# Kernel optimization log

Hardware: AMD Instinct MI355X
Metric: run time of the kernel (lower is better)

The kernel has to match this reference:

```python
import jax, jax.numpy as jnp
import numpy as np

B = 262144      # batch
DIN = 100       # input covariate dim (cfg_density[0][0])
H = 64          # hidden dim
G = 10          # num_grid -> density output dim G+1
NH = 5          # number of dosage-bucket heads in Multi_head


def setup_inputs() -> dict:
    key = jax.random.key(0)
    ks = jax.random.split(key, 16)
    s = 0.05
    return {
        "dosage": jax.random.uniform(ks[0], (B,), dtype=jnp.float32),
        "x": jax.random.normal(ks[1], (B, DIN), dtype=jnp.float32),
        # density feature MLP (two Linear+ReLU layers)
        "dW0": jax.random.normal(ks[2], (DIN, H), dtype=jnp.float32) * s,
        "db0": jax.random.normal(ks[3], (H,), dtype=jnp.float32) * s,
        "dW1": jax.random.normal(ks[4], (H, H), dtype=jnp.float32) * s,
        "db1": jax.random.normal(ks[5], (H,), dtype=jnp.float32) * s,
        # Density_Block: Linear(H -> G+1) then softmax + grid interpolation
        "dbW": jax.random.normal(ks[6], (H, G + 1), dtype=jnp.float32) * s,
        "dbB": jax.random.normal(ks[7], (G + 1,), dtype=jnp.float32) * s,
        # Multi_head: 5 structurally identical heads, params stacked on axis 0
        # layer0: Treat_Linear(64 -> 64, relu, istreat=1)
        "W0": jax.random.normal(ks[8], (NH, H, H), dtype=jnp.float32) * s,
        "tw0": jax.random.normal(ks[9], (NH, H), dtype=jnp.float32) * s,
        "b0": jax.random.normal(ks[10], (NH, H), dtype=jnp.float32) * s,
        # layer1 (last): Treat_Linear(64 -> 1, no act, istreat=1)
        "W1": jax.random.normal(ks[11], (NH, H, 1), dtype=jnp.float32) * s,
        "tw1": jax.random.normal(ks[12], (NH, 1), dtype=jnp.float32) * s,
        "b1": jax.random.normal(ks[13], (NH, 1), dtype=jnp.float32) * s,
    }


def reference(dosage, x, dW0, db0, dW1, db1, dbW, dbB, W0, tw0, b0, W1, tw1, b1):
    # hidden feature MLP
    hidden = jax.nn.relu(x @ dW0 + db0)
    hidden = jax.nn.relu(hidden @ dW1 + db1)            # [B, H]

    # ---- Density_Block: softmax over grid, dual gather + linear interpolation
    p = jax.nn.softmax(hidden @ dbW + dbB, axis=1)      # [B, G+1]
    tB = dosage * G
    U = jnp.ceil(tB)
    inter = 1.0 - (U - tB)                              # fractional position in cell
    Ui = U.astype(jnp.int32)
    Li = Ui - 1
    Li = Li + (Li < 0).astype(jnp.int32)                # clamp L=-1 -> 0
    pL = jnp.take_along_axis(p, Li[:, None], axis=1)[:, 0]
    pU = jnp.take_along_axis(p, Ui[:, None], axis=1)[:, 0]
    g = pL + (pU - pL) * inter                          # [B]

    # ---- Multi_head: 5 heads on dosage buckets [0,.2),[.2,.4),...,[.8,1.)
    t = dosage
    # layer0: out = feat @ W + t * tw + b, relu; compute all heads, select later
    h0 = jax.nn.relu(
        jnp.einsum('bi,hio->bho', hidden, W0)
        + t[:, None, None] * tw0[None]
        + b0[None]
    )                                                   # [B, NH, H]
    # last layer: no activation
    out1 = (jnp.einsum('bho,hoj->bhj', h0, W1)
            + t[:, None, None] * tw1[None]
            + b1[None])                                 # [B, NH, 1]
    bucket = jnp.clip(jnp.floor(t * NH).astype(jnp.int32), 0, NH - 1)
    Q = jnp.take_along_axis(out1, bucket[:, None, None], axis=1)[:, 0, :]  # [B, 1]
    return g, Q
```

## Files before the change

### kernel.cpp

```cpp
#include <hip/hip_runtime.h>

typedef __attribute__((ext_vector_type(8))) short  short8;
typedef __attribute__((ext_vector_type(4))) float  floatx4;
typedef __attribute__((ext_vector_type(4))) int    intx4;

constexpr int DIN = 100;
constexpr int H   = 64;
constexpr int G   = 10;
constexpr int NH  = 5;
constexpr int MWG = 128;
constexpr int HP  = 72;

constexpr int NF_DW0 = 16, NF_DW1 = 8, NF_DBW = 2;
constexpr int NF_LIN = NF_DW0 + NF_DW1 + NF_DBW;
constexpr int NF_TOT = NF_LIN + 40;

__device__ __forceinline__ unsigned short f2bf_rne(float f) {
    union { float f; unsigned u; } v{f};
    unsigned r = v.u + 0x7FFF + ((v.u >> 16) & 1);
    return (unsigned short)(r >> 16);
}

__device__ __forceinline__ short8 pack8(const float* f) {
    intx4 p;
    #pragma unroll
    for (int j = 0; j < 4; ++j) {
        unsigned a = __float_as_uint(f[2 * j])     + 0x8000u;
        unsigned b = __float_as_uint(f[2 * j + 1]) + 0x8000u;
        p[j] = (int)((b & 0xFFFF0000u) | (a >> 16));
    }
    union { intx4 i; short8 s; } u; u.i = p;
    return u.s;
}

__device__ __forceinline__ unsigned short f2bf_hu(float f) {
    return (unsigned short)((__float_as_uint(f) + 0x8000u) >> 16);
}

__device__ __forceinline__ short8 ldfrag(const unsigned short* __restrict__ ws,
                                         int f, int lane) {
    return *(const short8*)(ws + (size_t)(f * 64 + lane) * 8);
}

__global__ __launch_bounds__(64) void pack_kernel(
    const float* __restrict__ dW0, const float* __restrict__ dW1,
    const float* __restrict__ dbW, const float* __restrict__ W0,
    unsigned short* __restrict__ ws)
{
    const int f = blockIdx.x;
    const int lane = threadIdx.x;
    const int q = lane >> 4, cl = lane & 15;
    float v[8];
    if (f < NF_DW0) {
        int c = f >> 2, g = f & 3;
        #pragma unroll
        for (int j = 0; j < 8; ++j) {
            int k = c * 32 + q * 8 + j, n = g * 16 + cl;
            v[j] = (k < DIN) ? dW0[k * H + n] : 0.0f;
        }
    } else if (f < NF_DW0 + NF_DW1) {
        int r = f - NF_DW0; int c = r >> 2, g = r & 3;
        #pragma unroll
        for (int j = 0; j < 8; ++j) {
            int k = c * 32 + q * 8 + j, n = g * 16 + cl;
            v[j] = dW1[k * H + n];
        }
    } else if (f < NF_LIN) {
        int c = f - (NF_DW0 + NF_DW1);
        #pragma unroll
        for (int j = 0; j < 8; ++j) {
            int k = c * 32 + q * 8 + j, n = cl;
            v[j] = (n <= G) ? dbW[k * (G + 1) + n] : 0.0f;
        }
    } else {
        int r = f - NF_LIN; int h = r >> 3; r &= 7; int c = r >> 2, g = r & 3;
        #pragma unroll
        for (int j = 0; j < 8; ++j) {
            int k = c * 32 + q * 8 + j, n = g * 16 + cl;
            v[j] = W0[(h * H + k) * H + n];
        }
    }
    short8 s;
    #pragma unroll
    for (int j = 0; j < 8; ++j) s[j] = (short)f2bf_rne(v[j]);
    *(short8*)(ws + (size_t)(f * 64 + lane) * 8) = s;
}

__global__ __launch_bounds__(256, 3) void drnet_mfma(
    const float* __restrict__ dosage, const float* __restrict__ x,
    const float* __restrict__ db0, const float* __restrict__ db1,
    const float* __restrict__ dbB,
    const float* __restrict__ tw0, const float* __restrict__ b0,
    const float* __restrict__ W1, const float* __restrict__ tw1,
    const float* __restrict__ b1,
    const unsigned short* __restrict__ wsfrag,
    float* __restrict__ outg, float* __restrict__ outq)
{
    __shared__ unsigned short hbuf[MWG * HP];
    __shared__ int            perm[MWG];
    __shared__ float          tbuf[MWG];
    __shared__ unsigned char  bkbuf[MWG];
    __shared__ float          qbuf[MWG];
    __shared__ int            hist[NH];
    __shared__ int            offs[NH];

    const int tid  = threadIdx.x;
    const int wave = tid >> 6, lane = tid & 63;
    const int q = lane >> 4, cl = lane & 15;
    const int rowbase = blockIdx.x * MWG + wave * 32;
    unsigned short* hb = hbuf + wave * 32 * HP;

    if (tid < NH) hist[tid] = 0;
    __syncthreads();
    {
        float t8[2][4];
        int   bk8[2][4];
        #pragma unroll
        for (int mt = 0; mt < 2; ++mt) {
            floatx4 tv = *(const floatx4*)(dosage + rowbase + mt * 16 + 4 * q);
            #pragma unroll
            for (int r = 0; r < 4; ++r) {
                float t = tv[r];
                t8[mt][r] = t;
                int bk = (int)floorf(t * (float)NH);
                bk8[mt][r] = min(max(bk, 0), NH - 1);
            }
        }
        if (cl == 0) {
            #pragma unroll
            for (int mt = 0; mt < 2; ++mt)
                #pragma unroll
                for (int r = 0; r < 4; ++r)
                    atomicAdd(&hist[bk8[mt][r]], 1);
        }
        __syncthreads();
        if (tid == 0) {
            int a = 0;
            #pragma unroll
            for (int h = 0; h < NH; ++h) { offs[h] = a; a += hist[h]; }
        }
        __syncthreads();
        if (cl == 0) {
            #pragma unroll
            for (int mt = 0; mt < 2; ++mt)
                #pragma unroll
                for (int r = 0; r < 4; ++r) {
                    const int bk  = bk8[mt][r];
                    const int pos = atomicAdd(&offs[bk], 1);
                    perm[pos]  = wave * 32 + mt * 16 + 4 * q + r;
                    tbuf[pos]  = t8[mt][r];
                    bkbuf[pos] = (unsigned char)bk;
                }
        }
    }

    #pragma unroll 1
    for (int mt = 0; mt < 2; ++mt) {
        short8 a1[4];
        const float* xr = x + (size_t)(rowbase + mt * 16 + cl) * DIN;
        #pragma unroll
        for (int cch = 0; cch < 4; ++cch) {
            float f[8];
            if (cch < 3) {
                floatx4 u0 = *(const floatx4*)(xr + cch * 32 + q * 8);
                floatx4 u1 = *(const floatx4*)(xr + cch * 32 + q * 8 + 4);
                f[0]=u0.x; f[1]=u0.y; f[2]=u0.z; f[3]=u0.w;
                f[4]=u1.x; f[5]=u1.y; f[6]=u1.z; f[7]=u1.w;
            } else {
                if (q == 0) {
                    floatx4 u0 = *(const floatx4*)(xr + 96);
                    f[0]=u0.x; f[1]=u0.y; f[2]=u0.z; f[3]=u0.w;
                    f[4]=f[5]=f[6]=f[7]=0.0f;
                } else {
                    #pragma unroll
                    for (int j = 0; j < 8; ++j) f[j] = 0.0f;
                }
            }
            a1[cch] = pack8(f);
        }
        floatx4 acc[4];
        #pragma unroll
        for (int g = 0; g < 4; ++g) acc[g] = (floatx4)0.0f;
        #pragma unroll
        for (int cch = 0; cch < 4; ++cch)
            #pragma unroll
            for (int g = 0; g < 4; ++g) {
                short8 bf = ldfrag(wsfrag, cch * 4 + g, lane);
                acc[g] = __builtin_amdgcn_mfma_f32_16x16x32_bf16(a1[cch], bf, acc[g], 0, 0, 0);
            }
        #pragma unroll
        for (int g = 0; g < 4; ++g) {
            float bias = db0[g * 16 + cl];
            #pragma unroll
            for (int r = 0; r < 4; ++r)
                hb[(mt * 16 + 4 * q + r) * HP + g * 16 + cl] =
                    f2bf_hu(fmaxf(acc[g][r] + bias, 0.0f));
        }
    }

    #pragma unroll 1
    for (int mt = 0; mt < 2; ++mt) {
        short8 a2[2];
        #pragma unroll
        for (int cch = 0; cch < 2; ++cch)
            a2[cch] = *(const short8*)(hb + (mt * 16 + cl) * HP + cch * 32 + q * 8);
        floatx4 acc[4];
        #pragma unroll
        for (int g = 0; g < 4; ++g) acc[g] = (floatx4)0.0f;
        #pragma unroll
        for (int cch = 0; cch < 2; ++cch)
            #pragma unroll
            for (int g = 0; g < 4; ++g) {
                short8 bf = ldfrag(wsfrag, NF_DW0 + cch * 4 + g, lane);
                acc[g] = __builtin_amdgcn_mfma_f32_16x16x32_bf16(a2[cch], bf, acc[g], 0, 0, 0);
            }
        #pragma unroll
        for (int g = 0; g < 4; ++g) {
            float bias = db1[g * 16 + cl];
            #pragma unroll
            for (int r = 0; r < 4; ++r)
                hb[(mt * 16 + 4 * q + r) * HP + g * 16 + cl] =
                    f2bf_hu(fmaxf(acc[g][r] + bias, 0.0f));
        }
    }

    short8 af[2][2];
    #pragma unroll
    for (int mt = 0; mt < 2; ++mt)
        #pragma unroll
        for (int cch = 0; cch < 2; ++cch)
            af[mt][cch] = *(const short8*)(hb + (mt * 16 + cl) * HP + cch * 32 + q * 8);

    {
        floatx4 accd[2];
        accd[0] = (floatx4)0.0f; accd[1] = (floatx4)0.0f;
        #pragma unroll
        for (int cch = 0; cch < 2; ++cch) {
            short8 bf = ldfrag(wsfrag, NF_DW0 + NF_DW1 + cch, lane);
            #pragma unroll
            for (int mt = 0; mt < 2; ++mt)
                accd[mt] = __builtin_amdgcn_mfma_f32_16x16x32_bf16(af[mt][cch], bf, accd[mt], 0, 0, 0);
        }
        const float dbBv = (cl <= G) ? dbB[cl] : 0.0f;
        #pragma unroll
        for (int mt = 0; mt < 2; ++mt) {
            floatx4 tv = *(const floatx4*)(dosage + rowbase + mt * 16 + 4 * q);
            float gout[4];
            #pragma unroll
            for (int r = 0; r < 4; ++r) {
                float e = (cl <= G) ? __expf(accd[mt][r] + dbBv) : 0.0f;
                float s = e;
                s += __shfl_xor(s, 1); s += __shfl_xor(s, 2);
                s += __shfl_xor(s, 4); s += __shfl_xor(s, 8);
                const float t  = tv[r];
                const float tB = t * (float)G;
                const float U  = ceilf(tB);
                const float inter = 1.0f - (U - tB);
                int Ui = (int)U; int Li = Ui - 1; if (Li < 0) Li = 0;
                float pL = __shfl(e, q * 16 + Li);
                float pU = __shfl(e, q * 16 + Ui);
                gout[r] = (pL + (pU - pL) * inter) / s;
            }
            if (cl == 0) {
                floatx4 gv = { gout[0], gout[1], gout[2], gout[3] };
                *(floatx4*)(outg + rowbase + mt * 16 + 4 * q) = gv;
            }
        }
    }

    __syncthreads();
    #pragma unroll 1
    for (int mt = 0; mt < 2; ++mt) {
        const int base = (wave * 2 + mt) * 16;
        const int prow = perm[base + cl];
        short8 ag[2];
        ag[0] = *(const short8*)(hbuf + prow * HP + q * 8);
        ag[1] = *(const short8*)(hbuf + prow * HP + 32 + q * 8);
        floatx4 tv = *(const floatx4*)(tbuf + base + 4 * q);
        const unsigned bku = *(const unsigned*)(bkbuf + base + 4 * q);
        const int blo = bkbuf[base], bhi = bkbuf[base + 15];
        float qp4[4] = {0.0f, 0.0f, 0.0f, 0.0f};
        #pragma unroll 1
        for (int h = blo; h <= bhi; ++h) {
            floatx4 acch[4];
            #pragma unroll
            for (int g = 0; g < 4; ++g) acch[g] = (floatx4)0.0f;
            #pragma unroll
            for (int cch = 0; cch < 2; ++cch)
                #pragma unroll
                for (int g = 0; g < 4; ++g) {
                    short8 bf = ldfrag(wsfrag, NF_LIN + h * 8 + cch * 4 + g, lane);
                    acch[g] = __builtin_amdgcn_mfma_f32_16x16x32_bf16(ag[cch], bf, acch[g], 0, 0, 0);
                }
            #pragma unroll
            for (int g = 0; g < 4; ++g) {
                const int off = h * H + g * 16 + cl;
                const float tw0v = tw0[off], b0v = b0[off], w1v = W1[off];
                #pragma unroll
                for (int r = 0; r < 4; ++r) {
                    float h0 = acch[g][r] + tv[r] * tw0v + b0v;
                    float c  = fmaxf(h0, 0.0f) * w1v;
                    qp4[r] += (((bku >> (8 * r)) & 0xFFu) == (unsigned)h) ? c : 0.0f;
                }
            }
        }
        #pragma unroll
        for (int r = 0; r < 4; ++r) {
            float s = qp4[r];
            s += __shfl_xor(s, 1); s += __shfl_xor(s, 2);
            s += __shfl_xor(s, 4); s += __shfl_xor(s, 8);
            if (cl == 0) {
                const int bk = (int)((bku >> (8 * r)) & 0xFFu);
                qbuf[perm[base + 4 * q + r]] = s + tv[r] * tw1[bk] + b1[bk];
            }
        }
    }

    __syncthreads();
    if (tid < MWG / 4) {
        floatx4 v = *(const floatx4*)(qbuf + tid * 4);
        *(floatx4*)(outq + blockIdx.x * MWG + tid * 4) = v;
    }
}

extern "C" void kernel_launch(void* const* d_in, const int* in_sizes, int n_in,
                              void* d_out, int out_size, void* d_ws, size_t ws_size,
                              hipStream_t stream) {
    const float* dosage = (const float*)d_in[0];
    const float* x      = (const float*)d_in[1];
    const float* dW0    = (const float*)d_in[2];
    const float* db0    = (const float*)d_in[3];
    const float* dW1    = (const float*)d_in[4];
    const float* db1    = (const float*)d_in[5];
    const float* dbW    = (const float*)d_in[6];
    const float* dbB    = (const float*)d_in[7];
    const float* W0     = (const float*)d_in[8];
    const float* tw0    = (const float*)d_in[9];
    const float* b0     = (const float*)d_in[10];
    const float* W1     = (const float*)d_in[11];
    const float* tw1    = (const float*)d_in[12];
    const float* b1     = (const float*)d_in[13];

    const int Btot = in_sizes[0];
    float* outg = (float*)d_out;
    float* outq = outg + Btot;
    unsigned short* ws = (unsigned short*)d_ws;

    pack_kernel<<<NF_TOT, 64, 0, stream>>>(dW0, dW1, dbW, W0, ws);
    drnet_mfma<<<Btot / MWG, 256, 0, stream>>>(dosage, x, db0, db1, dbB,
                                               tw0, b0, W1, tw1, b1,
                                               ws, outg, outq);
}
```

Before: 196.3 us.

## Swap MFMA operands to transpose accumulator layout and simplify epilogues

The MFMA A/B operands are swapped so each lane owns one batch row with four consecutive output columns. Bias-add and ReLU epilogues can then write packed bf16 pairs as 8-byte LDS stores and load biases as float4. The softmax reduction needs only two cross-quad shuffles, and the grid gather goes through a small LDS buffer instead of per-element shuffles. The head epilogue is predicated per lane on its bucket with vectorised parameter loads, which cuts shuffle and scalar-store overhead. In exchange it adds LDS traffic for pbuf and introduces divergence on the bucket branch.

```diff
diff --git a/kernel.cpp b/kernel.cpp
--- a/kernel.cpp
+++ b/kernel.cpp
@@ -10,6 +10,7 @@
 constexpr int NH  = 5;
 constexpr int MWG = 128;
 constexpr int HP  = 72;
+constexpr int PBP = 20;
 
 constexpr int NF_DW0 = 16, NF_DW1 = 8, NF_DBW = 2;
 constexpr int NF_LIN = NF_DW0 + NF_DW1 + NF_DBW;
@@ -33,8 +34,10 @@
     return u.s;
 }
 
-__device__ __forceinline__ unsigned short f2bf_hu(float f) {
-    return (unsigned short)((__float_as_uint(f) + 0x8000u) >> 16);
+__device__ __forceinline__ unsigned pack2bf(float a, float b) {
+    unsigned ua = __float_as_uint(a) + 0x8000u;
+    unsigned ub = __float_as_uint(b) + 0x8000u;
+    return (ua >> 16) | (ub & 0xFFFF0000u);
 }
 
 __device__ __forceinline__ short8 ldfrag(const unsigned short* __restrict__ ws,
@@ -97,6 +100,7 @@
     float* __restrict__ outg, float* __restrict__ outq)
 {
     __shared__ unsigned short hbuf[MWG * HP];
+    __shared__ float          pbuf[4][16][PBP];
     __shared__ int            perm[MWG];
     __shared__ float          tbuf[MWG];
     __shared__ unsigned char  bkbuf[MWG];
@@ -186,15 +190,17 @@
             #pragma unroll
             for (int g = 0; g < 4; ++g) {
                 short8 bf = ldfrag(wsfrag, cch * 4 + g, lane);
-                acc[g] = __builtin_amdgcn_mfma_f32_16x16x32_bf16(a1[cch], bf, acc[g], 0, 0, 0);
+                acc[g] = __builtin_amdgcn_mfma_f32_16x16x32_bf16(bf, a1[cch], acc[g], 0, 0, 0);
             }
         #pragma unroll
         for (int g = 0; g < 4; ++g) {
-            float bias = db0[g * 16 + cl];
-            #pragma unroll
-            for (int r = 0; r < 4; ++r)
-                hb[(mt * 16 + 4 * q + r) * HP + g * 16 + cl] =
-                    f2bf_hu(fmaxf(acc[g][r] + bias, 0.0f));
+            floatx4 bias = *(const floatx4*)(db0 + g * 16 + 4 * q);
+            float v0 = fmaxf(acc[g][0] + bias[0], 0.0f);
+            float v1 = fmaxf(acc[g][1] + bias[1], 0.0f);
+            float v2 = fmaxf(acc[g][2] + bias[2], 0.0f);
+            float v3 = fmaxf(acc[g][3] + bias[3], 0.0f);
+            *(uint2*)(hb + (size_t)(mt * 16 + cl) * HP + g * 16 + 4 * q) =
+                make_uint2(pack2bf(v0, v1), pack2bf(v2, v3));
         }
     }
 
@@ -212,15 +218,17 @@
             #pragma unroll
             for (int g = 0; g < 4; ++g) {
                 short8 bf = ldfrag(wsfrag, NF_DW0 + cch * 4 + g, lane);
-                acc[g] = __builtin_amdgcn_mfma_f32_16x16x32_bf16(a2[cch], bf, acc[g], 0, 0, 0);
+                acc[g] = __builtin_amdgcn_mfma_f32_16x16x32_bf16(bf, a2[cch], acc[g], 0, 0, 0);
             }
         #pragma unroll
         for (int g = 0; g < 4; ++g) {
-            float bias = db1[g * 16 + cl];
-            #pragma unroll
-            for (int r = 0; r < 4; ++r)
-                hb[(mt * 16 + 4 * q + r) * HP + g * 16 + cl] =
-                    f2bf_hu(fmaxf(acc[g][r] + bias, 0.0f));
+            floatx4 bias = *(const floatx4*)(db1 + g * 16 + 4 * q);
+            float v0 = fmaxf(acc[g][0] + bias[0], 0.0f);
+            float v1 = fmaxf(acc[g][1] + bias[1], 0.0f);
+            float v2 = fmaxf(acc[g][2] + bias[2], 0.0f);
+            float v3 = fmaxf(acc[g][3] + bias[3], 0.0f);
+            *(uint2*)(hb + (size_t)(mt * 16 + cl) * HP + g * 16 + 4 * q) =
+                make_uint2(pack2bf(v0, v1), pack2bf(v2, v3));
         }
     }
 
@@ -239,32 +247,31 @@
             short8 bf = ldfrag(wsfrag, NF_DW0 + NF_DW1 + cch, lane);
             #pragma unroll
             for (int mt = 0; mt < 2; ++mt)
-                accd[mt] = __builtin_amdgcn_mfma_f32_16x16x32_bf16(af[mt][cch], bf, accd[mt], 0, 0, 0);
-        }
-        const float dbBv = (cl <= G) ? dbB[cl] : 0.0f;
+                accd[mt] = __builtin_amdgcn_mfma_f32_16x16x32_bf16(bf, af[mt][cch], accd[mt], 0, 0, 0);
+        }
         #pragma unroll
         for (int mt = 0; mt < 2; ++mt) {
-            floatx4 tv = *(const floatx4*)(dosage + rowbase + mt * 16 + 4 * q);
-            float gout[4];
+            floatx4 ev;
+            float sp = 0.0f;
             #pragma unroll
             for (int r = 0; r < 4; ++r) {
-                float e = (cl <= G) ? __expf(accd[mt][r] + dbBv) : 0.0f;
-                float s = e;
-                s += __shfl_xor(s, 1); s += __shfl_xor(s, 2);
-                s += __shfl_xor(s, 4); s += __shfl_xor(s, 8);
-                const float t  = tv[r];
-                const float tB = t * (float)G;
-                const float U  = ceilf(tB);
-                const float inter = 1.0f - (U - tB);
-                int Ui = (int)U; int Li = Ui - 1; if (Li < 0) Li = 0;
-                float pL = __shfl(e, q * 16 + Li);
-                float pU = __shfl(e, q * 16 + Ui);
-                gout[r] = (pL + (pU - pL) * inter) / s;
-            }
-            if (cl == 0) {
-                floatx4 gv = { gout[0], gout[1], gout[2], gout[3] };
-                *(floatx4*)(outg + rowbase + mt * 16 + 4 * q) = gv;
-            }
+                const int gd = 4 * q + r;
+                float e = (gd <= G) ? __expf(accd[mt][r] + dbB[gd]) : 0.0f;
+                ev[r] = e;
+                sp += e;
+            }
+            float s = sp;
+            s += __shfl_xor(s, 16); s += __shfl_xor(s, 32);
+            *(floatx4*)(&pbuf[wave][cl][4 * q]) = ev;
+            const float t  = dosage[rowbase + mt * 16 + cl];
+            const float tB = t * (float)G;
+            const float U  = ceilf(tB);
+            const float inter = 1.0f - (U - tB);
+            int Ui = (int)U; int Li = Ui - 1; if (Li < 0) Li = 0;
+            const float pL = pbuf[wave][cl][Li];
+            const float pU = pbuf[wave][cl][Ui];
+            if (q == 0)
+                outg[rowbase + mt * 16 + cl] = (pL + (pU - pL) * inter) / s;
         }
     }
 
@@ -276,10 +283,10 @@
         short8 ag[2];
         ag[0] = *(const short8*)(hbuf + prow * HP + q * 8);
         ag[1] = *(const short8*)(hbuf + prow * HP + 32 + q * 8);
-        floatx4 tv = *(const floatx4*)(tbuf + base + 4 * q);
-        const unsigned bku = *(const unsigned*)(bkbuf + base + 4 * q);
-        const int blo = bkbuf[base], bhi = bkbuf[base + 15];
-        float qp4[4] = {0.0f, 0.0f, 0.0f, 0.0f};
+        const float tme  = tbuf[base + cl];
+        const int   bkme = bkbuf[base + cl];
+        const int   blo  = bkbuf[base], bhi = bkbuf[base + 15];
+        float qp = 0.0f;
         #pragma unroll 1
         for (int h = blo; h <= bhi; ++h) {
             floatx4 acch[4];
@@ -290,30 +297,24 @@
                 #pragma unroll
                 for (int g = 0; g < 4; ++g) {
                     short8 bf = ldfrag(wsfrag, NF_LIN + h * 8 + cch * 4 + g, lane);
-                    acch[g] = __builtin_amdgcn_mfma_f32_16x16x32_bf16(ag[cch], bf, acch[g], 0, 0, 0);
+                    acch[g] = __builtin_amdgcn_mfma_f32_16x16x32_bf16(bf, ag[cch], acch[g], 0, 0, 0);
                 }
-            #pragma unroll
-            for (int g = 0; g < 4; ++g) {
-                const int off = h * H + g * 16 + cl;
-                const float tw0v = tw0[off], b0v = b0[off], w1v = W1[off];
+            if (bkme == h) {
                 #pragma unroll
-                for (int r = 0; r < 4; ++r) {
-                    float h0 = acch[g][r] + tv[r] * tw0v + b0v;
-                    float c  = fmaxf(h0, 0.0f) * w1v;
-                    qp4[r] += (((bku >> (8 * r)) & 0xFFu) == (unsigned)h) ? c : 0.0f;
+                for (int g = 0; g < 4; ++g) {
+                    const int off = h * H + g * 16 + 4 * q;
+                    floatx4 tw0v = *(const floatx4*)(tw0 + off);
+                    floatx4 b0v  = *(const floatx4*)(b0  + off);
+                    floatx4 w1v  = *(const floatx4*)(W1  + off);
+                    #pragma unroll
+                    for (int r = 0; r < 4; ++r)
+                        qp += fmaxf(acch[g][r] + tme * tw0v[r] + b0v[r], 0.0f) * w1v[r];
                 }
             }
         }
-        #pragma unroll
-        for (int r = 0; r < 4; ++r) {
-            float s = qp4[r];
-            s += __shfl_xor(s, 1); s += __shfl_xor(s, 2);
-            s += __shfl_xor(s, 4); s += __shfl_xor(s, 8);
-            if (cl == 0) {
-                const int bk = (int)((bku >> (8 * r)) & 0xFFu);
-                qbuf[perm[base + 4 * q + r]] = s + tv[r] * tw1[bk] + b1[bk];
-            }
-        }
+        qp += __shfl_xor(qp, 16); qp += __shfl_xor(qp, 32);
+        if (q == 0)
+            qbuf[prow] = qp + tme * tw1[bkme] + b1[bkme];
     }
 
     __syncthreads();
```

After: 204.7 us. +4.3%, slower.
